# Kernel optimization log

Measured on AMD Instinct MI355X. Metric: run time of the kernel, lower is better.

The kernel has to match this reference:

```python
import jax, jax.numpy as jnp
import numpy as np

K, N, GROUP = 4096, 12288, 64
M = 4096  # tokens (batch*seq)


def setup_inputs() -> dict:
    key = jax.random.key(0)
    k1, k2, k3, k4, k5 = jax.random.split(key, 5)
    input = jax.random.normal(k1, (M, K), dtype=jnp.float32)
    qweight = jax.random.randint(k2, (K, N), 0, 4, dtype=jnp.int32)  # int2 codes in [0,4)
    scale = jax.random.uniform(k3, (K // GROUP, N), dtype=jnp.float32)
    zp = jax.random.normal(k4, (K // GROUP, N), dtype=jnp.float32)
    bias = jax.random.normal(k5, (N,), dtype=jnp.float32)
    return {"input": input, "qweight": qweight, "scale": scale, "zp": zp, "bias": bias}


def reference(input, qweight, scale, zp, bias):
    # Group-wise asymmetric dequant: W[k,n] = q[k,n]*scale[k//g,n] + zp[k//g,n]
    G = K // GROUP
    q = qweight.astype(input.dtype).reshape(G, GROUP, N)
    w = q * scale[:, None, :] + zp[:, None, :]          # [G, g, N]
    w = w.reshape(K, N)
    out = input @ w + bias[None, :]                      # [M, N]
    return out
```

## Files before the change

kernel.cpp:

```cpp
#include <hip/hip_runtime.h>
#include <hip/hip_bf16.h>

#define Mdim 4096
#define Kdim 4096
#define Ndim 12288

typedef __attribute__((ext_vector_type(8))) short short8;
typedef __attribute__((ext_vector_type(4))) float floatx4;
typedef __attribute__((ext_vector_type(4))) int intx4;
typedef __attribute__((ext_vector_type(4))) unsigned short ushortx4;
typedef __attribute__((ext_vector_type(8))) unsigned short ushortx8;

static __device__ __forceinline__ unsigned short f2bf(float x) {
    __hip_bfloat16 h = __float2bfloat16(x);
    return __builtin_bit_cast(unsigned short, h);
}

static __device__ __forceinline__ void gload_lds16(const unsigned short* g, unsigned short* l) {
    __builtin_amdgcn_global_load_lds(
        (const __attribute__((address_space(1))) unsigned int*)g,
        (__attribute__((address_space(3))) unsigned int*)l,
        16, 0, 0);
}

__global__ void __launch_bounds__(256)
dequant_transpose(const int* __restrict__ Q, const float* __restrict__ S,
                  const float* __restrict__ Z, unsigned short* __restrict__ Wt)
{
    __shared__ unsigned short Ls[64][72];
    const int t     = threadIdx.x;
    const int kbase = blockIdx.x * 256;
    const int n0    = blockIdx.y * 64;
    const int tn = t & 15, tk = t >> 4;
    const int nc = tn * 4;
    const int n_out  = t >> 2;
    const int kc_out = (t & 3) * 16;

    #pragma unroll
    for (int s = 0; s < 4; ++s) {
        const int k0 = kbase + s * 64;
        const int g  = k0 >> 6;
        const floatx4 s4 = *reinterpret_cast<const floatx4*>(&S[(size_t)g * Ndim + n0 + nc]);
        const floatx4 z4 = *reinterpret_cast<const floatx4*>(&Z[(size_t)g * Ndim + n0 + nc]);
        intx4 q[4];
        #pragma unroll
        for (int r = 0; r < 4; ++r)
            q[r] = *reinterpret_cast<const intx4*>(&Q[(size_t)(k0 + tk * 4 + r) * Ndim + n0 + nc]);
        if (s) __syncthreads();
        #pragma unroll
        for (int j = 0; j < 4; ++j) {
            const float sv = s4[j], zv = z4[j];
            ushortx4 w;
            w.x = f2bf(fmaf((float)q[0][j], sv, zv));
            w.y = f2bf(fmaf((float)q[1][j], sv, zv));
            w.z = f2bf(fmaf((float)q[2][j], sv, zv));
            w.w = f2bf(fmaf((float)q[3][j], sv, zv));
            *reinterpret_cast<ushortx4*>(&Ls[nc + j][tk * 4]) = w;
        }
        __syncthreads();
        const ushortx8 a = *reinterpret_cast<const ushortx8*>(&Ls[n_out][kc_out]);
        const ushortx8 b = *reinterpret_cast<const ushortx8*>(&Ls[n_out][kc_out + 8]);
        unsigned short* dst = &Wt[(size_t)(n0 + n_out) * Kdim + k0 + kc_out];
        *reinterpret_cast<ushortx8*>(dst)     = a;
        *reinterpret_cast<ushortx8*>(dst + 8) = b;
    }
}

__global__ void __launch_bounds__(256)
xconv(const float* __restrict__ X, unsigned short* __restrict__ Xw)
{
    const size_t i = ((size_t)blockIdx.x * 256 + threadIdx.x) * 8;
    const floatx4 a = *reinterpret_cast<const floatx4*>(&X[i]);
    const floatx4 b = *reinterpret_cast<const floatx4*>(&X[i + 4]);
    ushortx8 w;
    w[0] = f2bf(a.x); w[1] = f2bf(a.y); w[2] = f2bf(a.z); w[3] = f2bf(a.w);
    w[4] = f2bf(b.x); w[5] = f2bf(b.y); w[6] = f2bf(b.z); w[7] = f2bf(b.w);
    *reinterpret_cast<ushortx8*>(&Xw[i]) = w;
}

__global__ void __launch_bounds__(256)
gemm_bf16(const unsigned short* __restrict__ A, const unsigned short* __restrict__ B,
          const float* __restrict__ bias, float* __restrict__ O)
{
    __shared__ unsigned short As[128 * 64];
    __shared__ unsigned short Bs[128 * 64];

    const int nblk = Ndim / 128;
    const int gsz  = 8 * nblk;
    const int grp  = blockIdx.x / gsz;
    const int r    = blockIdx.x % gsz;
    const int m0   = (grp * 8 + (r & 7)) * 128;
    const int n0   = (r >> 3) * 128;

    const int t    = threadIdx.x;
    const int wave = t >> 6;
    const int lane = t & 63;
    const int wm   = (wave & 1) * 64;
    const int wn   = (wave >> 1) * 64;
    const int lrow = lane & 15;
    const int quad = lane >> 4;
    const int lsw  = lrow & 7;

    const int srow = lane >> 3;
    const int scol = ((lane & 7) ^ srow) * 8;
    const unsigned short* Ag = &A[(size_t)(m0 + wave * 32 + srow) * Kdim + scol];
    const unsigned short* Bg = &B[(size_t)(n0 + wave * 32 + srow) * Kdim + scol];
    unsigned short* AsB = &As[(wave * 32) * 64];
    unsigned short* BsB = &Bs[(wave * 32) * 64];

    floatx4 acc[4][4];
    #pragma unroll
    for (int i = 0; i < 4; ++i)
        #pragma unroll
        for (int j = 0; j < 4; ++j)
            acc[i][j] = floatx4{0.f, 0.f, 0.f, 0.f};

    for (int k0 = 0; k0 < Kdim; k0 += 64) {
        #pragma unroll
        for (int it = 0; it < 4; ++it) {
            gload_lds16(Ag + (size_t)(it * 8) * Kdim + k0, AsB + it * 8 * 64);
            gload_lds16(Bg + (size_t)(it * 8) * Kdim + k0, BsB + it * 8 * 64);
        }
        __syncthreads();

        #pragma unroll
        for (int kk = 0; kk < 64; kk += 32) {
            const int cphys = (((kk >> 3) + quad) ^ lsw) * 8;
            short8 af[4], bfr[4];
            #pragma unroll
            for (int i = 0; i < 4; ++i)
                af[i] = *reinterpret_cast<const short8*>(
                    &As[(wm + i * 16 + lrow) * 64 + cphys]);
            #pragma unroll
            for (int j = 0; j < 4; ++j)
                bfr[j] = *reinterpret_cast<const short8*>(
                    &Bs[(wn + j * 16 + lrow) * 64 + cphys]);
            #pragma unroll
            for (int i = 0; i < 4; ++i)
                #pragma unroll
                for (int j = 0; j < 4; ++j)
                    acc[i][j] = __builtin_amdgcn_mfma_f32_16x16x32_bf16(
                        af[i], bfr[j], acc[i][j], 0, 0, 0);
        }
        __syncthreads();
    }

    #pragma unroll
    for (int j = 0; j < 4; ++j) {
        const int col = n0 + wn + j * 16 + lrow;
        const float bv = bias[col];
        #pragma unroll
        for (int i = 0; i < 4; ++i) {
            const int rbase = m0 + wm + i * 16 + quad * 4;
            #pragma unroll
            for (int rr = 0; rr < 4; ++rr)
                O[(size_t)(rbase + rr) * Ndim + col] = acc[i][j][rr] + bv;
        }
    }
}

__global__ void __launch_bounds__(256)
w2a16_gemm_fb(const float* __restrict__ X, const int* __restrict__ Q,
              const float* __restrict__ S, const float* __restrict__ Z,
              const float* __restrict__ bias, float* __restrict__ O)
{
    __shared__ unsigned short As[128][72];
    __shared__ unsigned short Bs[128][72];
    const int t  = threadIdx.x;
    const int n0 = blockIdx.x * 128;
    const int m0 = blockIdx.y * 128;
    const int wave = t >> 6, lane = t & 63;
    const int wm = (wave & 1) * 64, wn = (wave >> 1) * 64;
    const int lrow = lane & 15, quad = lane >> 4;
    floatx4 acc[4][4];
    #pragma unroll
    for (int i = 0; i < 4; ++i)
        #pragma unroll
        for (int j = 0; j < 4; ++j) acc[i][j] = floatx4{0.f, 0.f, 0.f, 0.f};
    const int a_row0 = t >> 4, a_c = (t & 15) * 4;
    const int b_n = t & 127, b_k0 = (t >> 7) * 32;
    for (int k0 = 0; k0 < Kdim; k0 += 64) {
        #pragma unroll
        for (int i = 0; i < 8; ++i) {
            const int row = a_row0 + i * 16;
            const floatx4 v = *reinterpret_cast<const floatx4*>(
                &X[(size_t)(m0 + row) * Kdim + k0 + a_c]);
            ushortx4 w;
            w.x = f2bf(v.x); w.y = f2bf(v.y); w.z = f2bf(v.z); w.w = f2bf(v.w);
            *reinterpret_cast<ushortx4*>(&As[row][a_c]) = w;
        }
        const int g = k0 >> 6;
        const float s = S[(size_t)g * Ndim + n0 + b_n];
        const float z = Z[(size_t)g * Ndim + n0 + b_n];
        #pragma unroll
        for (int i = 0; i < 8; ++i) {
            const int kk = b_k0 + i * 4;
            const int* qp = &Q[(size_t)(k0 + kk) * Ndim + n0 + b_n];
            ushortx4 w;
            w.x = f2bf(fmaf((float)qp[0],                s, z));
            w.y = f2bf(fmaf((float)qp[(size_t)Ndim],     s, z));
            w.z = f2bf(fmaf((float)qp[(size_t)2 * Ndim], s, z));
            w.w = f2bf(fmaf((float)qp[(size_t)3 * Ndim], s, z));
            *reinterpret_cast<ushortx4*>(&Bs[b_n][kk]) = w;
        }
        __syncthreads();
        #pragma unroll
        for (int kk = 0; kk < 64; kk += 32) {
            short8 af[4], bfr[4];
            #pragma unroll
            for (int i = 0; i < 4; ++i)
                af[i] = *reinterpret_cast<const short8*>(&As[wm + i * 16 + lrow][kk + quad * 8]);
            #pragma unroll
            for (int j = 0; j < 4; ++j)
                bfr[j] = *reinterpret_cast<const short8*>(&Bs[wn + j * 16 + lrow][kk + quad * 8]);
            #pragma unroll
            for (int i = 0; i < 4; ++i)
                #pragma unroll
                for (int j = 0; j < 4; ++j)
                    acc[i][j] = __builtin_amdgcn_mfma_f32_16x16x32_bf16(af[i], bfr[j], acc[i][j], 0, 0, 0);
        }
        __syncthreads();
    }
    #pragma unroll
    for (int j = 0; j < 4; ++j) {
        const int col = n0 + wn + j * 16 + lrow;
        const float bv = bias[col];
        #pragma unroll
        for (int i = 0; i < 4; ++i) {
            const int rbase = m0 + wm + i * 16 + quad * 4;
            #pragma unroll
            for (int rr = 0; rr < 4; ++rr)
                O[(size_t)(rbase + rr) * Ndim + col] = acc[i][j][rr] + bv;
        }
    }
}

extern "C" void kernel_launch(void* const* d_in, const int* in_sizes, int n_in,
                              void* d_out, int out_size, void* d_ws, size_t ws_size,
                              hipStream_t stream) {
    const float* X  = (const float*)d_in[0];
    const int*   Q  = (const int*)d_in[1];
    const float* S  = (const float*)d_in[2];
    const float* Z  = (const float*)d_in[3];
    const float* Bi = (const float*)d_in[4];
    float* O = (float*)d_out;

    const size_t wt_bytes = (size_t)Kdim * Ndim * 2;
    const size_t xw_bytes = (size_t)Mdim * Kdim * 2;

    if (ws_size >= wt_bytes + xw_bytes) {
        unsigned short* Wt = (unsigned short*)d_ws;
        unsigned short* Xw = (unsigned short*)((char*)d_ws + wt_bytes);

        dim3 g1(Kdim / 256, Ndim / 64);
        hipLaunchKernelGGL(dequant_transpose, g1, dim3(256), 0, stream, Q, S, Z, Wt);

        const int xblocks = (Mdim * Kdim) / (256 * 8);
        hipLaunchKernelGGL(xconv, dim3(xblocks), dim3(256), 0, stream, X, Xw);

        const int nblocks = (Mdim / 128) * (Ndim / 128);
        hipLaunchKernelGGL(gemm_bf16, dim3(nblocks), dim3(256), 0, stream, Xw, Wt, Bi, O);
    } else {
        dim3 grid(Ndim / 128, Mdim / 128);
        hipLaunchKernelGGL(w2a16_gemm_fb, grid, dim3(256), 0, stream, X, Q, S, Z, Bi, O);
    }
}
```

Measured before the change: 863.5 us.

## Rewrite bf16 GEMM as 256x256 tile, 8-wave, double-buffered phased pipeline

Replaces the 128x128 single-buffered GEMM with a 256x256 tile using 512 threads and double-buffered LDS. Global-to-LDS loads for the next K tiles are interleaved with MFMA phases under explicit barriers, waitcnts and raised priority. An XCD-aware block swizzle is also added. The aim is to hide load latency and raise arithmetic intensity, at the cost of 128KB LDS per block and heavy register pressure from the 8x4 accumulator.

```diff
diff --git a/kernel.cpp b/kernel.cpp
--- a/kernel.cpp
+++ b/kernel.cpp
@@ -78,71 +78,129 @@
     *reinterpret_cast<ushortx8*>(&Xw[i]) = w;
 }
 
-__global__ void __launch_bounds__(256)
-gemm_bf16(const unsigned short* __restrict__ A, const unsigned short* __restrict__ B,
-          const float* __restrict__ bias, float* __restrict__ O)
+
+#define STAGE_A(c, kt, h) do { \
+    const unsigned short* sp_ = A + aoff + (size_t)((h) * 128) * Kdim + (size_t)(kt) * 64; \
+    unsigned short* dp_ = &As[c][((h) * 128 + wave * 16) * 64]; \
+    gload_lds16(sp_, dp_); \
+    gload_lds16(sp_ + (size_t)8 * Kdim, dp_ + 8 * 64); \
+} while (0)
+
+#define STAGE_B(c, kt, h) do { \
+    const unsigned short* sp_ = B + boff + (size_t)((h) * 128) * Kdim + (size_t)(kt) * 64; \
+    unsigned short* dp_ = &Bs[c][((h) * 128 + wave * 16) * 64]; \
+    gload_lds16(sp_, dp_); \
+    gload_lds16(sp_ + (size_t)8 * Kdim, dp_ + 8 * 64); \
+} while (0)
+
+#define LDA_(c, i, kh) (*reinterpret_cast<const short8*>( \
+    &As[c][(wm + (i) * 16 + lrow) * 64 + (((kh) * 4 + quad) ^ lsw) * 8]))
+#define LDB_(c, j, kh) (*reinterpret_cast<const short8*>( \
+    &Bs[c][(wn + (j) * 16 + lrow) * 64 + (((kh) * 4 + quad) ^ lsw) * 8]))
+
+#define PHASE_SYNC() do { \
+    __builtin_amdgcn_s_barrier(); \
+    asm volatile("s_waitcnt lgkmcnt(0)" ::: "memory"); \
+    __builtin_amdgcn_sched_barrier(0); \
+} while (0)
+
+#define MFMA_QUAD(ILO, JO) do { \
+    __builtin_amdgcn_s_setprio(1); \
+    _Pragma("unroll") \
+    for (int i_ = 0; i_ < 4; ++i_) { \
+        _Pragma("unroll") \
+        for (int jj_ = 0; jj_ < 2; ++jj_) { \
+            acc[(ILO) + i_][(JO) + jj_] = __builtin_amdgcn_mfma_f32_16x16x32_bf16( \
+                af[(ILO) + i_][0], bfr[jj_][0], acc[(ILO) + i_][(JO) + jj_], 0, 0, 0); \
+            acc[(ILO) + i_][(JO) + jj_] = __builtin_amdgcn_mfma_f32_16x16x32_bf16( \
+                af[(ILO) + i_][1], bfr[jj_][1], acc[(ILO) + i_][(JO) + jj_], 0, 0, 0); \
+        } \
+    } \
+    __builtin_amdgcn_s_setprio(0); \
+} while (0)
+
+__global__ void __launch_bounds__(512, 2)
+gemm_bf16_8p(const unsigned short* __restrict__ A, const unsigned short* __restrict__ B,
+             const float* __restrict__ bias, float* __restrict__ O)
 {
-    __shared__ unsigned short As[128 * 64];
-    __shared__ unsigned short Bs[128 * 64];
-
-    const int nblk = Ndim / 128;
+    __shared__ unsigned short As[2][256 * 64];
+    __shared__ unsigned short Bs[2][256 * 64];
+
+    constexpr int NT = Kdim / 64;
+
+    const int nblk = Ndim / 256;
+    const int cpx  = (Mdim / 256) * nblk / 8;
+    const int bid  = blockIdx.x;
+    const int swz  = (bid & 7) * cpx + (bid >> 3);
     const int gsz  = 8 * nblk;
-    const int grp  = blockIdx.x / gsz;
-    const int r    = blockIdx.x % gsz;
-    const int m0   = (grp * 8 + (r & 7)) * 128;
-    const int n0   = (r >> 3) * 128;
+    const int grp  = swz / gsz;
+    const int r    = swz % gsz;
+    const int m0   = (grp * 8 + (r & 7)) * 256;
+    const int n0   = (r >> 3) * 256;
 
     const int t    = threadIdx.x;
     const int wave = t >> 6;
     const int lane = t & 63;
-    const int wm   = (wave & 1) * 64;
-    const int wn   = (wave >> 1) * 64;
+    const int wm   = (wave >> 2) * 128;
+    const int wn   = (wave & 3) * 64;
     const int lrow = lane & 15;
     const int quad = lane >> 4;
     const int lsw  = lrow & 7;
 
     const int srow = lane >> 3;
     const int scol = ((lane & 7) ^ srow) * 8;
-    const unsigned short* Ag = &A[(size_t)(m0 + wave * 32 + srow) * Kdim + scol];
-    const unsigned short* Bg = &B[(size_t)(n0 + wave * 32 + srow) * Kdim + scol];
-    unsigned short* AsB = &As[(wave * 32) * 64];
-    unsigned short* BsB = &Bs[(wave * 32) * 64];
-
-    floatx4 acc[4][4];
-    #pragma unroll
-    for (int i = 0; i < 4; ++i)
+    const size_t aoff = (size_t)(m0 + wave * 16 + srow) * Kdim + scol;
+    const size_t boff = (size_t)(n0 + wave * 16 + srow) * Kdim + scol;
+
+    floatx4 acc[8][4];
+    #pragma unroll
+    for (int i = 0; i < 8; ++i)
         #pragma unroll
         for (int j = 0; j < 4; ++j)
             acc[i][j] = floatx4{0.f, 0.f, 0.f, 0.f};
 
-    for (int k0 = 0; k0 < Kdim; k0 += 64) {
-        #pragma unroll
-        for (int it = 0; it < 4; ++it) {
-            gload_lds16(Ag + (size_t)(it * 8) * Kdim + k0, AsB + it * 8 * 64);
-            gload_lds16(Bg + (size_t)(it * 8) * Kdim + k0, BsB + it * 8 * 64);
-        }
-        __syncthreads();
-
-        #pragma unroll
-        for (int kk = 0; kk < 64; kk += 32) {
-            const int cphys = (((kk >> 3) + quad) ^ lsw) * 8;
-            short8 af[4], bfr[4];
-            #pragma unroll
-            for (int i = 0; i < 4; ++i)
-                af[i] = *reinterpret_cast<const short8*>(
-                    &As[(wm + i * 16 + lrow) * 64 + cphys]);
-            #pragma unroll
-            for (int j = 0; j < 4; ++j)
-                bfr[j] = *reinterpret_cast<const short8*>(
-                    &Bs[(wn + j * 16 + lrow) * 64 + cphys]);
-            #pragma unroll
-            for (int i = 0; i < 4; ++i)
-                #pragma unroll
-                for (int j = 0; j < 4; ++j)
-                    acc[i][j] = __builtin_amdgcn_mfma_f32_16x16x32_bf16(
-                        af[i], bfr[j], acc[i][j], 0, 0, 0);
-        }
-        __syncthreads();
+    short8 af[8][2];
+    short8 bfr[2][2];
+
+    STAGE_A(0, 0, 0); STAGE_A(0, 0, 1);
+    STAGE_B(0, 0, 0); STAGE_B(0, 0, 1);
+    STAGE_A(1, 1, 0); STAGE_A(1, 1, 1);
+    asm volatile("s_waitcnt vmcnt(4)" ::: "memory");
+    __builtin_amdgcn_s_barrier();
+    __builtin_amdgcn_sched_barrier(0);
+
+    for (int u = 0; u < NT; ++u) {
+        const int c = u & 1;
+
+        #pragma unroll
+        for (int i = 0; i < 4; ++i) { af[i][0] = LDA_(c, i, 0); af[i][1] = LDA_(c, i, 1); }
+        #pragma unroll
+        for (int j = 0; j < 2; ++j) { bfr[j][0] = LDB_(c, j, 0); bfr[j][1] = LDB_(c, j, 1); }
+        if (u + 1 < NT) STAGE_B(c ^ 1, u + 1, 0);
+        PHASE_SYNC();
+        MFMA_QUAD(0, 0);
+        __builtin_amdgcn_s_barrier();
+
+        #pragma unroll
+        for (int i = 4; i < 8; ++i) { af[i][0] = LDA_(c, i, 0); af[i][1] = LDA_(c, i, 1); }
+        if (u + 1 < NT) STAGE_B(c ^ 1, u + 1, 1);
+        PHASE_SYNC();
+        MFMA_QUAD(4, 0);
+        __builtin_amdgcn_s_barrier();
+
+        #pragma unroll
+        for (int j = 0; j < 2; ++j) { bfr[j][0] = LDB_(c, j + 2, 0); bfr[j][1] = LDB_(c, j + 2, 1); }
+        if (u + 2 < NT) STAGE_A(c, u + 2, 0);
+        PHASE_SYNC();
+        MFMA_QUAD(0, 2);
+        __builtin_amdgcn_s_barrier();
+
+        if (u + 2 < NT) STAGE_A(c, u + 2, 1);
+        MFMA_QUAD(4, 2);
+        if (u < NT - 2) { asm volatile("s_waitcnt vmcnt(4)" ::: "memory"); }
+        else            { asm volatile("s_waitcnt vmcnt(0)" ::: "memory"); }
+        __builtin_amdgcn_s_barrier();
+        __builtin_amdgcn_sched_barrier(0);
     }
 
     #pragma unroll
@@ -150,7 +208,7 @@
         const int col = n0 + wn + j * 16 + lrow;
         const float bv = bias[col];
         #pragma unroll
-        for (int i = 0; i < 4; ++i) {
+        for (int i = 0; i < 8; ++i) {
             const int rbase = m0 + wm + i * 16 + quad * 4;
             #pragma unroll
             for (int rr = 0; rr < 4; ++rr)
@@ -164,8 +222,8 @@
               const float* __restrict__ S, const float* __restrict__ Z,
               const float* __restrict__ bias, float* __restrict__ O)
 {
-    __shared__ unsigned short As[128][72];
-    __shared__ unsigned short Bs[128][72];
+    __shared__ unsigned short Asf[128][72];
+    __shared__ unsigned short Bsf[128][72];
     const int t  = threadIdx.x;
     const int n0 = blockIdx.x * 128;
     const int m0 = blockIdx.y * 128;
@@ -187,7 +245,7 @@
                 &X[(size_t)(m0 + row) * Kdim + k0 + a_c]);
             ushortx4 w;
             w.x = f2bf(v.x); w.y = f2bf(v.y); w.z = f2bf(v.z); w.w = f2bf(v.w);
-            *reinterpret_cast<ushortx4*>(&As[row][a_c]) = w;
+            *reinterpret_cast<ushortx4*>(&Asf[row][a_c]) = w;
         }
         const int g = k0 >> 6;
         const float s = S[(size_t)g * Ndim + n0 + b_n];
@@ -201,23 +259,23 @@
             w.y = f2bf(fmaf((float)qp[(size_t)Ndim],     s, z));
             w.z = f2bf(fmaf((float)qp[(size_t)2 * Ndim], s, z));
             w.w = f2bf(fmaf((float)qp[(size_t)3 * Ndim], s, z));
-            *reinterpret_cast<ushortx4*>(&Bs[b_n][kk]) = w;
+            *reinterpret_cast<ushortx4*>(&Bsf[b_n][kk]) = w;
         }
         __syncthreads();
         #pragma unroll
         for (int kk = 0; kk < 64; kk += 32) {
-            short8 af[4], bfr[4];
+            short8 afv[4], bfv[4];
             #pragma unroll
             for (int i = 0; i < 4; ++i)
-                af[i] = *reinterpret_cast<const short8*>(&As[wm + i * 16 + lrow][kk + quad * 8]);
+                afv[i] = *reinterpret_cast<const short8*>(&Asf[wm + i * 16 + lrow][kk + quad * 8]);
             #pragma unroll
             for (int j = 0; j < 4; ++j)
-                bfr[j] = *reinterpret_cast<const short8*>(&Bs[wn + j * 16 + lrow][kk + quad * 8]);
+                bfv[j] = *reinterpret_cast<const short8*>(&Bsf[wn + j * 16 + lrow][kk + quad * 8]);
             #pragma unroll
             for (int i = 0; i < 4; ++i)
                 #pragma unroll
                 for (int j = 0; j < 4; ++j)
-                    acc[i][j] = __builtin_amdgcn_mfma_f32_16x16x32_bf16(af[i], bfr[j], acc[i][j], 0, 0, 0);
+                    acc[i][j] = __builtin_amdgcn_mfma_f32_16x16x32_bf16(afv[i], bfv[j], acc[i][j], 0, 0, 0);
         }
         __syncthreads();
     }
@@ -258,8 +316,8 @@
         const int xblocks = (Mdim * Kdim) / (256 * 8);
         hipLaunchKernelGGL(xconv, dim3(xblocks), dim3(256), 0, stream, X, Xw);
 
-        const int nblocks = (Mdim / 128) * (Ndim / 128);
-        hipLaunchKernelGGL(gemm_bf16, dim3(nblocks), dim3(256), 0, stream, Xw, Wt, Bi, O);
+        const int nblocks = (Mdim / 256) * (Ndim / 256);
+        hipLaunchKernelGGL(gemm_bf16_8p, dim3(nblocks), dim3(512), 0, stream, Xw, Wt, Bi, O);
     } else {
         dim3 grid(Ndim / 128, Mdim / 128);
         hipLaunchKernelGGL(w2a16_gemm_fb, grid, dim3(256), 0, stream, X, Q, S, Z, Bi, O);
```

Measured after the change: 790.6 us. -8.4%, faster.
